# Optimization experiments

Measured on AMD Instinct MI355X. Metric: run time of the kernel, lower is better.

The kernel has to match this reference:

```python
import jax, jax.numpy as jnp
import numpy as np

N, D, K = 131072, 64, 4096


def setup_inputs() -> dict:
    key = jax.random.key(0)
    k1, k2 = jax.random.split(key)
    x = jax.random.normal(k1, (N, D), dtype=jnp.float32)
    embed = jax.random.normal(k2, (K, D), dtype=jnp.float32)
    return {"x": x, "embed": embed}


def reference(x, embed):
    """EuclideanCodebook forward.

    x:     [N, D] flat input vectors
    embed: [K, D] codebook
    Returns (quantize [N,D], embed_ind [N], cluster_size [K], embed_sum [K,D]).
    cluster_size / embed_sum are the one-hot scatter statistics fed to the
    EMA codebook update (embed_onehot.sum(0) and flatten^T @ embed_onehot).
    """
    num_codes = embed.shape[0]
    x2 = jnp.sum(x * x, axis=-1, keepdims=True)               # [N, 1]
    e2 = jnp.sum(embed * embed, axis=-1)                      # [K]
    dist = x2 - 2.0 * (x @ embed.T) + e2[None, :]             # [N, K]
    embed_ind = jnp.argmin(dist, axis=-1)                     # [N]
    quantize = embed[embed_ind]                               # gather [N, D]
    # scatter statistics for EMA update
    cluster_size = jnp.zeros((num_codes,), x.dtype).at[embed_ind].add(1.0)  # [K]
    embed_sum = jax.ops.segment_sum(x, embed_ind, num_segments=num_codes)   # [K, D]
    return quantize, embed_ind, cluster_size, embed_sum
```

## Files before the change

### kernel.cpp

```cpp
#include <hip/hip_runtime.h>

#define N_ROWS 131072
#define DIM 64
#define K_CODES 4096
#define BROWS 256
#define CK 64
#define NCH (K_CODES / CK)
#define EST 72
#define EPS 0.015625f

typedef __attribute__((ext_vector_type(8))) short short8;
typedef __attribute__((ext_vector_type(4))) float f32x4;

__device__ inline unsigned short bf16rn(float f) {
    unsigned int u = __float_as_uint(f);
    u += 0x7FFFu + ((u >> 16) & 1u);
    return (unsigned short)(u >> 16);
}
__device__ inline unsigned int fkey(float f) {
    unsigned int u = __float_as_uint(f);
    return (u & 0x80000000u) ? ~u : (u | 0x80000000u);
}

__global__ void e2_kernel(const float* __restrict__ embed, float* __restrict__ e2) {
    int k = blockIdx.x * blockDim.x + threadIdx.x;
    const float4* e = reinterpret_cast<const float4*>(embed + (size_t)k * DIM);
    float s = 0.f;
#pragma unroll
    for (int i = 0; i < DIM / 4; ++i) {
        float4 v = e[i];
        s = fmaf(v.x, v.x, s);
        s = fmaf(v.y, v.y, s);
        s = fmaf(v.z, v.z, s);
        s = fmaf(v.w, v.w, s);
    }
    e2[k] = s;
}

__global__ void pack_kernel(const float* __restrict__ embed,
                            unsigned short* __restrict__ ebf) {
    const int g = blockIdx.x * blockDim.x + threadIdx.x;
    const int code = g >> 4;
    const int w    = g & 15;
    const int half = w >> 3;
    const int d0   = (w & 7) << 3;
    const float* ep = embed + (size_t)code * DIM + d0;
    float4 f0 = *(const float4*)ep;
    float4 f1 = *(const float4*)(ep + 4);
    float wv[8] = {f0.x, f0.y, f0.z, f0.w, f1.x, f1.y, f1.z, f1.w};
    unsigned short o[8];
#pragma unroll
    for (int j = 0; j < 8; ++j) {
        unsigned short hb = bf16rn(wv[j]);
        if (half == 0) {
            o[j] = hb;
        } else {
            float hf = __uint_as_float(((unsigned int)hb) << 16);
            o[j] = bf16rn(wv[j] - hf);
        }
    }
    *(uint4*)(ebf + (size_t)code * 128 + half * 64 + d0) = *(uint4*)o;
}

__global__ __launch_bounds__(256, 2) void dist_argmin_kernel(
        const float* __restrict__ x, const unsigned short* __restrict__ ebf,
        const float* __restrict__ e2g, int* __restrict__ ind_ws,
        float* __restrict__ ind_out, int* __restrict__ cnt,
        int* __restrict__ list) {
    __shared__ unsigned short esh[CK * EST];
    __shared__ unsigned short esl[CK * EST];
    __shared__ float e2s[CK];

    const int tid  = threadIdx.x;
    const int l15  = tid & 15;
    const int quad = (tid >> 4) & 3;
    const int wave = tid >> 6;
    const int r0w  = blockIdx.x * BROWS + wave * 64;

    short8 ah[4][2], al[4][2];
#pragma unroll
    for (int i = 0; i < 4; ++i)
#pragma unroll
        for (int s = 0; s < 2; ++s) {
            const float* xp = x + (size_t)(r0w + 16 * i + l15) * DIM + 32 * s + 8 * quad;
            float4 f0 = *(const float4*)xp;
            float4 f1 = *(const float4*)(xp + 4);
            float w[8] = {f0.x, f0.y, f0.z, f0.w, f1.x, f1.y, f1.z, f1.w};
            short8 h, l;
#pragma unroll
            for (int j = 0; j < 8; ++j) {
                unsigned short hb = bf16rn(w[j]);
                float hf = __uint_as_float(((unsigned int)hb) << 16);
                h[j] = (short)hb;
                l[j] = (short)bf16rn(w[j] - hf);
            }
            ah[i][s] = h;
            al[i][s] = l;
        }

    float s1[16], s2[16];
    int c1[16];
#pragma unroll
    for (int t = 0; t < 16; ++t) { s1[t] = 3.4e38f; s2[t] = 3.4e38f; c1[t] = 0; }

    for (int ch = 0; ch < NCH; ++ch) {
        const int c0 = ch * CK;
        __syncthreads();
        {
            const int col = tid >> 2;
            const int dq  = (tid & 3) * 16;
            const unsigned short* pp = ebf + (size_t)(c0 + col) * 128 + dq;
            uint4 h0 = *(const uint4*)pp;
            uint4 h1 = *(const uint4*)(pp + 8);
            uint4 l0 = *(const uint4*)(pp + 64);
            uint4 l1 = *(const uint4*)(pp + 72);
            *(uint4*)(&esh[col * EST + dq])     = h0;
            *(uint4*)(&esh[col * EST + dq + 8]) = h1;
            *(uint4*)(&esl[col * EST + dq])     = l0;
            *(uint4*)(&esl[col * EST + dq + 8]) = l1;
            if (tid < CK) e2s[tid] = e2g[c0 + tid];
        }
        __syncthreads();

        f32x4 acc[4][4];
#pragma unroll
        for (int i = 0; i < 4; ++i)
#pragma unroll
            for (int j = 0; j < 4; ++j) acc[i][j] = (f32x4){0.f, 0.f, 0.f, 0.f};

#pragma unroll
        for (int j = 0; j < 4; ++j) {
            const int cb = (16 * j + l15) * EST + 8 * quad;
            short8 bh0 = *(const short8*)(&esh[cb]);
            short8 bh1 = *(const short8*)(&esh[cb + 32]);
            short8 bl0 = *(const short8*)(&esl[cb]);
            short8 bl1 = *(const short8*)(&esl[cb + 32]);
#pragma unroll
            for (int i = 0; i < 4; ++i) {
                f32x4 a = acc[i][j];
                a = __builtin_amdgcn_mfma_f32_16x16x32_bf16(ah[i][0], bh0, a, 0, 0, 0);
                a = __builtin_amdgcn_mfma_f32_16x16x32_bf16(ah[i][1], bh1, a, 0, 0, 0);
                a = __builtin_amdgcn_mfma_f32_16x16x32_bf16(ah[i][0], bl0, a, 0, 0, 0);
                a = __builtin_amdgcn_mfma_f32_16x16x32_bf16(ah[i][1], bl1, a, 0, 0, 0);
                a = __builtin_amdgcn_mfma_f32_16x16x32_bf16(al[i][0], bh0, a, 0, 0, 0);
                a = __builtin_amdgcn_mfma_f32_16x16x32_bf16(al[i][1], bh1, a, 0, 0, 0);
                acc[i][j] = a;
            }
        }

#pragma unroll
        for (int j = 0; j < 4; ++j) {
            const int c = c0 + 16 * j + l15;
            const float e2v = e2s[16 * j + l15];
#pragma unroll
            for (int i = 0; i < 4; ++i)
#pragma unroll
                for (int r = 0; r < 4; ++r) {
                    float sc = fmaf(-2.f, acc[i][j][r], e2v);
                    const int st = i * 4 + r;
                    bool lt = sc < s1[st];
                    s2[st] = lt ? s1[st] : fminf(s2[st], sc);
                    c1[st] = lt ? c : c1[st];
                    s1[st] = lt ? sc : s1[st];
                }
        }
    }

#pragma unroll
    for (int st = 0; st < 16; ++st) {
#pragma unroll
        for (int m = 1; m < 16; m <<= 1) {
            float os1 = __shfl_xor(s1[st], m, 64);
            float os2 = __shfl_xor(s2[st], m, 64);
            int   oc1 = __shfl_xor(c1[st], m, 64);
            bool take = (os1 < s1[st]) || (os1 == s1[st] && oc1 < c1[st]);
            float loser = take ? s1[st] : os1;
            s2[st] = fminf(fminf(s2[st], os2), loser);
            if (take) { s1[st] = os1; c1[st] = oc1; }
        }
    }
    if (l15 == 0) {
#pragma unroll
        for (int st = 0; st < 16; ++st) {
            const int i = st >> 2, r = st & 3;
            const int row = r0w + 16 * i + 4 * quad + r;
            ind_ws[row] = c1[st];
            ind_out[row] = (float)c1[st];
            if (s2[st] - s1[st] < EPS) {
                int p = atomicAdd(cnt, 1);
                list[p] = row;
            }
        }
    }
}

__global__ void refine_kernel(const float* __restrict__ x,
                              const float* __restrict__ embed,
                              const float* __restrict__ e2g,
                              const int* __restrict__ cnt,
                              const int* __restrict__ list,
                              int* __restrict__ ind_ws,
                              float* __restrict__ ind_out) {
    __shared__ float xr[DIM];
    __shared__ unsigned long long red[256];
    const int tid = threadIdx.x;
    const int n = *cnt;
    for (int f = blockIdx.x; f < n; f += gridDim.x) {
        const int row = list[f];
        __syncthreads();
        if (tid < 16)
            ((float4*)xr)[tid] = ((const float4*)(x + (size_t)row * DIM))[tid];
        __syncthreads();
        unsigned long long best = ~0ull;
        for (int c = tid; c < K_CODES; c += 256) {
            const float4* ep = (const float4*)(embed + (size_t)c * DIM);
            float d0 = 0.f, d1 = 0.f, d2 = 0.f, d3 = 0.f;
#pragma unroll
            for (int q = 0; q < 16; ++q) {
                float4 ev = ep[q];
                d0 = fmaf(xr[4 * q + 0], ev.x, d0);
                d1 = fmaf(xr[4 * q + 1], ev.y, d1);
                d2 = fmaf(xr[4 * q + 2], ev.z, d2);
                d3 = fmaf(xr[4 * q + 3], ev.w, d3);
            }
            float sc = fmaf(-2.f, (d0 + d1) + (d2 + d3), e2g[c]);
            unsigned long long key =
                ((unsigned long long)fkey(sc) << 32) | (unsigned int)c;
            if (key < best) best = key;
        }
        red[tid] = best;
        __syncthreads();
        for (int w = 128; w > 0; w >>= 1) {
            if (tid < w && red[tid + w] < red[tid]) red[tid] = red[tid + w];
            __syncthreads();
        }
        if (tid == 0) {
            int k = (int)(red[0] & 0xFFFFFFFFull);
            ind_ws[row] = k;
            ind_out[row] = (float)k;
        }
    }
}

__global__ void scatter_kernel(const float* __restrict__ x,
                               const float* __restrict__ embed,
                               const int* __restrict__ ind,
                               float* __restrict__ quant,
                               float* __restrict__ cs,
                               float* __restrict__ esum) {
    const int t = blockIdx.x * blockDim.x + threadIdx.x;
    const int row = t >> 6;
    const int d = t & 63;
    const int k = ind[row];
    quant[t] = embed[(size_t)k * DIM + d];
    atomicAdd(&esum[(size_t)k * DIM + d], x[t]);
    if (d == 0) atomicAdd(&cs[k], 1.0f);
}

extern "C" void kernel_launch(void* const* d_in, const int* in_sizes, int n_in,
                              void* d_out, int out_size, void* d_ws, size_t ws_size,
                              hipStream_t stream) {
    const float* x     = (const float*)d_in[0];
    const float* embed = (const float*)d_in[1];

    float* out     = (float*)d_out;
    float* quant   = out;
    float* ind_out = out + (size_t)N_ROWS * DIM;
    float* cs      = ind_out + N_ROWS;
    float* esum    = cs + K_CODES;

    float* e2   = (float*)d_ws;
    int* cnt    = (int*)(e2 + K_CODES);
    int* list   = cnt + 4;
    int* ind_ws = list + N_ROWS;

    unsigned short* ebf = (unsigned short*)quant;

    hipMemsetAsync(cs, 0, (size_t)(K_CODES + K_CODES * DIM) * sizeof(float), stream);
    hipMemsetAsync(cnt, 0, sizeof(int), stream);

    e2_kernel<<<K_CODES / 256, 256, 0, stream>>>(embed, e2);
    pack_kernel<<<(K_CODES * 16) / 256, 256, 0, stream>>>(embed, ebf);
    dist_argmin_kernel<<<N_ROWS / BROWS, 256, 0, stream>>>(
        x, ebf, e2, ind_ws, ind_out, cnt, list);
    refine_kernel<<<512, 256, 0, stream>>>(x, embed, e2, cnt, list, ind_ws, ind_out);
    scatter_kernel<<<(size_t)N_ROWS * DIM / 256, 256, 0, stream>>>(
        x, embed, ind_ws, quant, cs, esum);
}
```

Measured before the change: 451.7 us.

## Fold e2 into MFMA accumulator init and fuse prep kernels and memsets

The scoring is rewritten to maximize x·e - 0.5||e||^2. The -0.5·e2 term is preloaded into the MFMA accumulators, which removes the per-element fma in the argmin loop, and the top-two tracking switches to a cheaper fmax/fmin form with the ambiguity threshold halved to match. The e2 computation and both memsets are folded into pack_kernel, removing two launches and a memset. In exchange, pack_kernel takes on an extra strided zeroing loop, and the refine threshold semantics change slightly.

```diff
diff --git a/kernel.cpp b/kernel.cpp
--- a/kernel.cpp
+++ b/kernel.cpp
@@ -8,6 +8,7 @@
 #define NCH (K_CODES / CK)
 #define EST 72
 #define EPS 0.015625f
+#define HEPS 0.0078125f
 
 typedef __attribute__((ext_vector_type(8))) short short8;
 typedef __attribute__((ext_vector_type(4))) float f32x4;
@@ -22,24 +23,17 @@
     return (u & 0x80000000u) ? ~u : (u | 0x80000000u);
 }
 
-__global__ void e2_kernel(const float* __restrict__ embed, float* __restrict__ e2) {
-    int k = blockIdx.x * blockDim.x + threadIdx.x;
-    const float4* e = reinterpret_cast<const float4*>(embed + (size_t)k * DIM);
-    float s = 0.f;
-#pragma unroll
-    for (int i = 0; i < DIM / 4; ++i) {
-        float4 v = e[i];
-        s = fmaf(v.x, v.x, s);
-        s = fmaf(v.y, v.y, s);
-        s = fmaf(v.z, v.z, s);
-        s = fmaf(v.w, v.w, s);
-    }
-    e2[k] = s;
-}
-
 __global__ void pack_kernel(const float* __restrict__ embed,
-                            unsigned short* __restrict__ ebf) {
+                            unsigned short* __restrict__ ebf,
+                            float* __restrict__ e2,
+                            float* __restrict__ e2h,
+                            int* __restrict__ cnt,
+                            float* __restrict__ cs) {
     const int g = blockIdx.x * blockDim.x + threadIdx.x;
+    for (int i = g; i < K_CODES + K_CODES * DIM; i += K_CODES * 16)
+        cs[i] = 0.f;
+    if (g == 0) *cnt = 0;
+
     const int code = g >> 4;
     const int w    = g & 15;
     const int half = w >> 3;
@@ -49,22 +43,31 @@
     float4 f1 = *(const float4*)(ep + 4);
     float wv[8] = {f0.x, f0.y, f0.z, f0.w, f1.x, f1.y, f1.z, f1.w};
     unsigned short o[8];
+    float ssq = 0.f;
 #pragma unroll
     for (int j = 0; j < 8; ++j) {
         unsigned short hb = bf16rn(wv[j]);
         if (half == 0) {
             o[j] = hb;
+            ssq = fmaf(wv[j], wv[j], ssq);
         } else {
             float hf = __uint_as_float(((unsigned int)hb) << 16);
             o[j] = bf16rn(wv[j] - hf);
         }
     }
     *(uint4*)(ebf + (size_t)code * 128 + half * 64 + d0) = *(uint4*)o;
+    ssq += __shfl_xor(ssq, 1, 64);
+    ssq += __shfl_xor(ssq, 2, 64);
+    ssq += __shfl_xor(ssq, 4, 64);
+    if (w == 0) {
+        e2[code]  = ssq;
+        e2h[code] = -0.5f * ssq;
+    }
 }
 
 __global__ __launch_bounds__(256, 2) void dist_argmin_kernel(
         const float* __restrict__ x, const unsigned short* __restrict__ ebf,
-        const float* __restrict__ e2g, int* __restrict__ ind_ws,
+        const float* __restrict__ e2h, int* __restrict__ ind_ws,
         float* __restrict__ ind_out, int* __restrict__ cnt,
         int* __restrict__ list) {
     __shared__ unsigned short esh[CK * EST];
@@ -101,7 +104,7 @@
     float s1[16], s2[16];
     int c1[16];
 #pragma unroll
-    for (int t = 0; t < 16; ++t) { s1[t] = 3.4e38f; s2[t] = 3.4e38f; c1[t] = 0; }
+    for (int t = 0; t < 16; ++t) { s1[t] = -3.4e38f; s2[t] = -3.4e38f; c1[t] = 0; }
 
     for (int ch = 0; ch < NCH; ++ch) {
         const int c0 = ch * CK;
@@ -118,15 +121,18 @@
             *(uint4*)(&esh[col * EST + dq + 8]) = h1;
             *(uint4*)(&esl[col * EST + dq])     = l0;
             *(uint4*)(&esl[col * EST + dq + 8]) = l1;
-            if (tid < CK) e2s[tid] = e2g[c0 + tid];
+            if (tid < CK) e2s[tid] = e2h[c0 + tid];
         }
         __syncthreads();
 
         f32x4 acc[4][4];
 #pragma unroll
-        for (int i = 0; i < 4; ++i)
-#pragma unroll
-            for (int j = 0; j < 4; ++j) acc[i][j] = (f32x4){0.f, 0.f, 0.f, 0.f};
+        for (int j = 0; j < 4; ++j) {
+            const float ev = e2s[16 * j + l15];
+            const f32x4 iv = {ev, ev, ev, ev};
+#pragma unroll
+            for (int i = 0; i < 4; ++i) acc[i][j] = iv;
+        }
 
 #pragma unroll
         for (int j = 0; j < 4; ++j) {
@@ -151,17 +157,16 @@
 #pragma unroll
         for (int j = 0; j < 4; ++j) {
             const int c = c0 + 16 * j + l15;
-            const float e2v = e2s[16 * j + l15];
 #pragma unroll
             for (int i = 0; i < 4; ++i)
 #pragma unroll
                 for (int r = 0; r < 4; ++r) {
-                    float sc = fmaf(-2.f, acc[i][j][r], e2v);
+                    float d = acc[i][j][r];
                     const int st = i * 4 + r;
-                    bool lt = sc < s1[st];
-                    s2[st] = lt ? s1[st] : fminf(s2[st], sc);
-                    c1[st] = lt ? c : c1[st];
-                    s1[st] = lt ? sc : s1[st];
+                    bool gt = d > s1[st];
+                    s2[st] = fmaxf(fminf(d, s1[st]), s2[st]);
+                    c1[st] = gt ? c : c1[st];
+                    s1[st] = fmaxf(s1[st], d);
                 }
         }
     }
@@ -173,9 +178,9 @@
             float os1 = __shfl_xor(s1[st], m, 64);
             float os2 = __shfl_xor(s2[st], m, 64);
             int   oc1 = __shfl_xor(c1[st], m, 64);
-            bool take = (os1 < s1[st]) || (os1 == s1[st] && oc1 < c1[st]);
+            bool take = (os1 > s1[st]) || (os1 == s1[st] && oc1 < c1[st]);
             float loser = take ? s1[st] : os1;
-            s2[st] = fminf(fminf(s2[st], os2), loser);
+            s2[st] = fmaxf(fmaxf(s2[st], os2), loser);
             if (take) { s1[st] = os1; c1[st] = oc1; }
         }
     }
@@ -186,7 +191,7 @@
             const int row = r0w + 16 * i + 4 * quad + r;
             ind_ws[row] = c1[st];
             ind_out[row] = (float)c1[st];
-            if (s2[st] - s1[st] < EPS) {
+            if (s1[st] - s2[st] < HEPS) {
                 int p = atomicAdd(cnt, 1);
                 list[p] = row;
             }
@@ -273,16 +278,14 @@
     int* cnt    = (int*)(e2 + K_CODES);
     int* list   = cnt + 4;
     int* ind_ws = list + N_ROWS;
+    float* e2h  = (float*)(ind_ws + N_ROWS);
 
     unsigned short* ebf = (unsigned short*)quant;
 
-    hipMemsetAsync(cs, 0, (size_t)(K_CODES + K_CODES * DIM) * sizeof(float), stream);
-    hipMemsetAsync(cnt, 0, sizeof(int), stream);
-
-    e2_kernel<<<K_CODES / 256, 256, 0, stream>>>(embed, e2);
-    pack_kernel<<<(K_CODES * 16) / 256, 256, 0, stream>>>(embed, ebf);
+    pack_kernel<<<(K_CODES * 16) / 256, 256, 0, stream>>>(
+        embed, ebf, e2, e2h, cnt, cs);
     dist_argmin_kernel<<<N_ROWS / BROWS, 256, 0, stream>>>(
-        x, ebf, e2, ind_ws, ind_out, cnt, list);
+        x, ebf, e2h, ind_ws, ind_out, cnt, list);
     refine_kernel<<<512, 256, 0, stream>>>(x, embed, e2, cnt, list, ind_ws, ind_out);
     scatter_kernel<<<(size_t)N_ROWS * DIM / 256, 256, 0, stream>>>(
         x, embed, ind_ws, quant, cs, esum);
```

Result: no change. 443.3 us (-1.9%).
